# Performance work log

Measured on AMD Instinct MI355X. Metric: run time of the kernel, lower is better.

The kernel has to match this reference:

```python
import jax, jax.numpy as jnp
import numpy as np

LEAK = 0.01  # torch LeakyReLU default negative_slope

def lrelu(x):
    return jnp.where(x >= 0, x, LEAK * x)

def edge_conv(x, src, dst, ea, W1, b1, W2, b2):
    # message: cat(x_i=target, x_j=source, edge_attr) -> Linear -> LeakyReLU -> Linear
    m = jnp.concatenate([x[dst], x[src], ea], axis=1)          # [E, 2F+Fe]
    h = lrelu(m @ W1 + b1) @ W2 + b2                            # [E, H]
    n = x.shape[0]
    agg = jnp.full((n, h.shape[1]), jnp.inf, h.dtype).at[dst].min(h)  # scatter-min at target
    return jnp.where(jnp.isfinite(agg), agg, jnp.zeros_like(agg))     # empty nodes -> 0


def setup_inputs() -> dict:
    key = jax.random.key(0)
    ks = jax.random.split(key, 20)
    B, N, E = 4, 20000, 640000
    NF, AD, EF, H = 2, 1, 1, 8
    inp = {
        "node_features": jax.random.randint(ks[0], (B, N, NF), 0, 10, dtype=jnp.int32),
        "actions": jax.random.normal(ks[1], (B, N), dtype=jnp.float32),
        "edge_index": jax.random.randint(ks[2], (B, 2, E), 0, N, dtype=jnp.int64),
        "edge_features": jax.random.normal(ks[3], (B, E, EF), dtype=jnp.float32),
    }
    d0 = NF + AD  # 3
    def lin(k, fin, fout):
        s = 1.0 / np.sqrt(fin)
        k1, k2 = jax.random.split(k)
        return (jax.random.uniform(k1, (fin, fout), jnp.float32, -s, s),
                jax.random.uniform(k2, (fout,), jnp.float32, -s, s))
    inp["c1_W1"], inp["c1_b1"] = lin(ks[4], 2 * d0 + EF, H)
    inp["c1_W2"], inp["c1_b2"] = lin(ks[5], H, H)
    inp["c2_W1"], inp["c2_b1"] = lin(ks[6], 2 * H + 1, H)
    inp["c2_W2"], inp["c2_b2"] = lin(ks[7], H, H)
    inp["c3_W1"], inp["c3_b1"] = lin(ks[8], 2 * H + 1, H)
    inp["c3_W2"], inp["c3_b2"] = lin(ks[9], H, H)
    inp["lin_W"], inp["lin_b"] = lin(ks[10], d0 + H, 1)
    return inp


def reference(node_features, actions, edge_index, edge_features,
              c1_W1, c1_b1, c1_W2, c1_b2,
              c2_W1, c2_b1, c2_W2, c2_b2,
              c3_W1, c3_b1, c3_W2, c3_b2,
              lin_W, lin_b):
    # x = int(node_features) concat actions  -> float
    x0 = jnp.concatenate([node_features.astype(jnp.int32).astype(jnp.float32),
                          actions[..., None]], axis=-1)  # [B,N,3]

    def per_graph(x0g, eig, eag):
        src, dst = eig[0], eig[1]  # flow source_to_target: x_j=src, x_i=dst
        h = lrelu(edge_conv(x0g, src, dst, eag, c1_W1, c1_b1, c1_W2, c1_b2))
        h = lrelu(edge_conv(h, src, dst, eag, c2_W1, c2_b1, c2_W2, c2_b2))
        h = lrelu(edge_conv(h, src, dst, eag, c3_W1, c3_b1, c3_W2, c3_b2))
        xc = jnp.concatenate([x0g, h], axis=1)  # [N, 3+8]
        return jnp.sum(xc, axis=0)              # sum-pool over nodes

    pooled = jax.vmap(per_graph)(x0, edge_index, edge_features)  # [B, 11]
    return pooled @ lin_W + lin_b  # [B, 1]
```

## Files before the change

### kernel.cpp

```cpp
#include <hip/hip_runtime.h>

#define LEAK 0.01f
#define BS 128
#define PCHUNK 8192
#define PT 512
#define CT 512
#define MAXNB 1024

__device__ __forceinline__ float lrelu(float v) {
    return v >= 0.f ? v : LEAK * v;
}

__device__ __forceinline__ unsigned int fmin_encode(float x) {
    unsigned int u = __float_as_uint(x);
    return (u & 0x80000000u) ? ~u : (u | 0x80000000u);
}
__device__ __forceinline__ float fmin_decode(unsigned int k) {
    unsigned int u = (k & 0x80000000u) ? (k ^ 0x80000000u) : ~k;
    return __uint_as_float(u);
}

__device__ __forceinline__ void block_add(float c, float* dst) {
    __shared__ float wsum[8];
#pragma unroll
    for (int off = 32; off > 0; off >>= 1) c += __shfl_down(c, off, 64);
    int lane = threadIdx.x & 63;
    int wave = threadIdx.x >> 6;
    if (lane == 0) wsum[wave] = c;
    __syncthreads();
    if (threadIdx.x == 0) {
        float s = 0.f;
        int nw = blockDim.x >> 6;
        for (int w = 0; w < nw; ++w) s += wsum[w];
        atomicAdd(dst, s);
    }
}

__global__ __launch_bounds__(256) void init_pre1_kernel(
    const int* __restrict__ nf, const float* __restrict__ act,
    const float* __restrict__ W1, const float* __restrict__ b1,
    const float* __restrict__ lw, const float* __restrict__ lb,
    float* __restrict__ a1, float* __restrict__ a2,
    float* __restrict__ out, int N) {
    int b = blockIdx.y;
    int n = blockIdx.x * 256 + threadIdx.x;
    float c = 0.f;
    if (n < N) {
        size_t i = (size_t)b * N + n;
        float x0 = (float)nf[i * 2 + 0];
        float x1 = (float)nf[i * 2 + 1];
        float x2 = act[i];
        float v1[8], v2[8];
#pragma unroll
        for (int j = 0; j < 8; ++j) {
            v1[j] = b1[j] + x0 * W1[0 * 8 + j] + x1 * W1[1 * 8 + j] + x2 * W1[2 * 8 + j];
            v2[j] =         x0 * W1[3 * 8 + j] + x1 * W1[4 * 8 + j] + x2 * W1[5 * 8 + j];
        }
        float4* o1 = (float4*)(a1 + i * 8);
        float4* o2 = (float4*)(a2 + i * 8);
        o1[0] = make_float4(v1[0], v1[1], v1[2], v1[3]);
        o1[1] = make_float4(v1[4], v1[5], v1[6], v1[7]);
        o2[0] = make_float4(v2[0], v2[1], v2[2], v2[3]);
        o2[1] = make_float4(v2[4], v2[5], v2[6], v2[7]);
        c = x0 * lw[0] + x1 * lw[1] + x2 * lw[2];
        if (n == 0) c += lb[0];
    }
    block_add(c, &out[b]);
}


__global__ __launch_bounds__(PT) void bucket_hist_kernel(
    const int* __restrict__ ei, int* __restrict__ bcnt, int E, int NB) {
    __shared__ int lc[MAXNB];
    int b = blockIdx.y;
    int t = threadIdx.x;
    for (int i = t; i < NB; i += PT) lc[i] = 0;
    __syncthreads();
    int e0 = blockIdx.x * PCHUNK;
    int end = min(e0 + PCHUNK, E);
    const int* drow = ei + (size_t)b * 2 * E + E;
    for (int e = e0 + t; e < end; e += PT)
        atomicAdd(&lc[drow[e] >> 7], 1);
    __syncthreads();
    for (int i = t; i < NB; i += PT)
        if (lc[i]) atomicAdd(&bcnt[b * NB + i], lc[i]);
}

__global__ __launch_bounds__(1024) void bucket_scan_kernel(
    const int* __restrict__ bcnt, int* __restrict__ base,
    int* __restrict__ fill, int TB) {
    __shared__ int ts[1024];
    int t = threadIdx.x;
    int i0 = 2 * t, i1 = 2 * t + 1;
    int v0 = (i0 < TB) ? bcnt[i0] : 0;
    int v1 = (i1 < TB) ? bcnt[i1] : 0;
    int s = v0 + v1;
    ts[t] = s;
    __syncthreads();
    int incl = s;
    for (int off = 1; off < 1024; off <<= 1) {
        int add = (t >= off) ? ts[t - off] : 0;
        __syncthreads();
        incl += add;
        ts[t] = incl;
        __syncthreads();
    }
    int ex = incl - s;
    if (i0 < TB) { base[i0] = ex; fill[i0] = ex; }
    if (i1 < TB) { base[i1] = ex + v0; fill[i1] = ex + v0; }
    if (t == 0) base[TB] = ts[1023];
}

__global__ __launch_bounds__(PT) void part_kernel(
    const int* __restrict__ ei, const float* __restrict__ ea,
    int* __restrict__ fill, int2* __restrict__ pairs, int E, int NB) {
    __shared__ int lc[MAXNB];
    __shared__ int lbase[MAXNB];
    int b = blockIdx.y;
    int t = threadIdx.x;
    for (int i = t; i < NB; i += PT) lc[i] = 0;
    __syncthreads();
    int e0 = blockIdx.x * PCHUNK;
    int end = min(e0 + PCHUNK, E);
    const int* srow = ei + (size_t)b * 2 * E;
    const int* drow = srow + E;
    int pk[PCHUNK / PT];
#pragma unroll
    for (int j = 0; j < PCHUNK / PT; ++j) {
        int e = e0 + j * PT + t;
        int p = -1;
        if (e < end) {
            int d = drow[e];
            int bin = d >> 7;
            int r = atomicAdd(&lc[bin], 1);
            p = bin | ((d & 127) << 10) | (r << 17);
        }
        pk[j] = p;
    }
    __syncthreads();
    for (int i = t; i < NB; i += PT) {
        int c = lc[i];
        lbase[i] = c ? atomicAdd(&fill[b * NB + i], c) : 0;
    }
    __syncthreads();
#pragma unroll
    for (int j = 0; j < PCHUNK / PT; ++j) {
        int e = e0 + j * PT + t;
        if (e < end) {
            int p = pk[j];
            int bin = p & 1023;
            int dl = (p >> 10) & 127;
            int r = p >> 17;
            pairs[lbase[bin] + r] =
                make_int2(srow[e] | (dl << 16), __float_as_int(ea[(size_t)b * E + e]));
        }
    }
}


__device__ __forceinline__ void conv_edges(
    const float* __restrict__ a2g, const float* we, const float* bb,
    const float* __restrict__ W2, const int2* __restrict__ pairs,
    int k0, int k1, const float* __restrict__ a1s, unsigned int* __restrict__ acc) {
    int t = threadIdx.x;
    for (int k = k0 + t; k < k1; k += 2 * CT) {
        int2 p0 = pairs[k];
        bool has1 = (k + CT < k1);
        int2 p1 = has1 ? pairs[k + CT] : p0;
        const float4* q0 = (const float4*)(a2g + (size_t)(p0.x & 0xFFFF) * 8);
        float4 lo0 = q0[0], hi0 = q0[1];
        const float4* q1 = (const float4*)(a2g + (size_t)(p1.x & 0xFFFF) * 8);
        float4 lo1 = q1[0], hi1 = q1[1];
#pragma unroll
        for (int which = 0; which < 2; ++which) {
            if (which == 1 && !has1) break;
            int dl = ((which ? p1.x : p0.x) >> 16) & 127;
            float eav = __int_as_float(which ? p1.y : p0.y);
            float4 lo = which ? lo1 : lo0;
            float4 hi = which ? hi1 : hi0;
            float h1[8];
            h1[0] = a1s[dl * 9 + 0] + lo.x; h1[1] = a1s[dl * 9 + 1] + lo.y;
            h1[2] = a1s[dl * 9 + 2] + lo.z; h1[3] = a1s[dl * 9 + 3] + lo.w;
            h1[4] = a1s[dl * 9 + 4] + hi.x; h1[5] = a1s[dl * 9 + 5] + hi.y;
            h1[6] = a1s[dl * 9 + 6] + hi.z; h1[7] = a1s[dl * 9 + 7] + hi.w;
#pragma unroll
            for (int j = 0; j < 8; ++j) {
                h1[j] = fmaf(eav, we[j], h1[j]);
                h1[j] = lrelu(h1[j]);
            }
            float h2[8];
#pragma unroll
            for (int j = 0; j < 8; ++j) h2[j] = bb[j];
#pragma unroll
            for (int kk = 0; kk < 8; ++kk) {
                float hk = h1[kk];
#pragma unroll
                for (int j = 0; j < 8; ++j) h2[j] = fmaf(hk, W2[kk * 8 + j], h2[j]);
            }
#pragma unroll
            for (int j = 0; j < 8; ++j)
                atomicMin(&acc[dl * 9 + j], fmin_encode(h2[j]));
        }
    }
}

__global__ __launch_bounds__(CT) void conv_mid_kernel(
    const float* __restrict__ a1, const float* __restrict__ a2,
    const float* __restrict__ w1e, const float* __restrict__ W2,
    const float* __restrict__ b2,
    const float* __restrict__ nW1, const float* __restrict__ nb1,
    const int* __restrict__ base, const int2* __restrict__ pairs,
    float* __restrict__ na1, float* __restrict__ na2, int N, int NB) {
    __shared__ float a1s[BS * 9];
    __shared__ unsigned int acc[BS * 9];
    int b = blockIdx.y;
    int bkt = b * NB + blockIdx.x;
    int n0 = blockIdx.x << 7;
    int nCnt = min(BS, N - n0);
    int t = threadIdx.x;
    size_t gn0 = ((size_t)b * N + n0) * 8;

    for (int i = t; i < nCnt * 8; i += CT)
        a1s[(i >> 3) * 9 + (i & 7)] = a1[gn0 + i];
    for (int i = t; i < BS * 9; i += CT) acc[i] = 0xFFFFFFFFu;
    float we[8], bb[8];
#pragma unroll
    for (int j = 0; j < 8; ++j) { we[j] = w1e[j]; bb[j] = b2[j]; }
    __syncthreads();

    conv_edges(a2 + (size_t)b * N * 8, we, bb, W2, pairs, base[bkt], base[bkt + 1],
               a1s, acc);
    __syncthreads();

    for (int i = t; i < nCnt * 8; i += CT) {
        float v = fmin_decode(acc[(i >> 3) * 9 + (i & 7)]);
        unsigned int u = __float_as_uint(v);
        if ((u & 0x7F800000u) == 0x7F800000u) v = 0.f;
        a1s[(i >> 3) * 9 + (i & 7)] = lrelu(v);
    }
    __syncthreads();

    int node = t >> 1, half = t & 1;
    if (node < nCnt) {
        float h[8];
#pragma unroll
        for (int j = 0; j < 8; ++j) h[j] = a1s[node * 9 + j];
        float v[8];
#pragma unroll
        for (int j = 0; j < 8; ++j) v[j] = half ? 0.f : nb1[j];
        const float* Wbase = nW1 + (half ? 64 : 0);
#pragma unroll
        for (int k = 0; k < 8; ++k) {
            float hk = h[k];
#pragma unroll
            for (int j = 0; j < 8; ++j) v[j] = fmaf(hk, Wbase[k * 8 + j], v[j]);
        }
        float* dst = (half ? na2 : na1) + gn0 + (size_t)node * 8;
        float4* o = (float4*)dst;
        o[0] = make_float4(v[0], v[1], v[2], v[3]);
        o[1] = make_float4(v[4], v[5], v[6], v[7]);
    }
}

__global__ __launch_bounds__(CT) void conv_final_kernel(
    const float* __restrict__ a1, const float* __restrict__ a2,
    const float* __restrict__ w1e, const float* __restrict__ W2,
    const float* __restrict__ b2, const float* __restrict__ lw,
    const int* __restrict__ base, const int2* __restrict__ pairs,
    float* __restrict__ out, int N, int NB) {
    __shared__ float a1s[BS * 9];
    __shared__ unsigned int acc[BS * 9];
    int b = blockIdx.y;
    int bkt = b * NB + blockIdx.x;
    int n0 = blockIdx.x << 7;
    int nCnt = min(BS, N - n0);
    int t = threadIdx.x;
    size_t gn0 = ((size_t)b * N + n0) * 8;

    for (int i = t; i < nCnt * 8; i += CT)
        a1s[(i >> 3) * 9 + (i & 7)] = a1[gn0 + i];
    for (int i = t; i < BS * 9; i += CT) acc[i] = 0xFFFFFFFFu;
    float we[8], bb[8];
#pragma unroll
    for (int j = 0; j < 8; ++j) { we[j] = w1e[j]; bb[j] = b2[j]; }
    __syncthreads();

    conv_edges(a2 + (size_t)b * N * 8, we, bb, W2, pairs, base[bkt], base[bkt + 1],
               a1s, acc);
    __syncthreads();

    float c = 0.f;
    if (t < nCnt) {
#pragma unroll
        for (int j = 0; j < 8; ++j) {
            float v = fmin_decode(acc[t * 9 + j]);
            unsigned int u = __float_as_uint(v);
            if ((u & 0x7F800000u) == 0x7F800000u) v = 0.f;
            c = fmaf(lrelu(v), lw[3 + j], c);
        }
    }
    __syncthreads();
    block_add(c, &out[b]);
}


__global__ __launch_bounds__(256) void node_init_kernel(
    const int* __restrict__ nf, const float* __restrict__ act,
    float* __restrict__ x0, int BN) {
    int tid = blockIdx.x * blockDim.x + threadIdx.x;
    if (tid >= BN) return;
    x0[tid * 3 + 0] = (float)nf[tid * 2 + 0];
    x0[tid * 3 + 1] = (float)nf[tid * 2 + 1];
    x0[tid * 3 + 2] = act[tid];
}

template <int D>
__global__ __launch_bounds__(256) void edge_conv_kernel(
    const float* __restrict__ x, const int* __restrict__ ei,
    const float* __restrict__ ea,
    const float* __restrict__ W1, const float* __restrict__ b1,
    const float* __restrict__ W2, const float* __restrict__ b2,
    unsigned int* __restrict__ agg, int E, int N, int B) {
    int tid = blockIdx.x * blockDim.x + threadIdx.x;
    if (tid >= B * E) return;
    int b = tid / E;
    int e = tid - b * E;
    const int* eb = ei + (size_t)b * 2 * E;
    int s = eb[e];
    int d = eb[E + e];
    const float* xi = x + ((size_t)b * N + d) * D;
    const float* xj = x + ((size_t)b * N + s) * D;
    constexpr int M = 2 * D + 1;
    float m[M];
#pragma unroll
    for (int k = 0; k < D; ++k) { m[k] = xi[k]; m[D + k] = xj[k]; }
    m[2 * D] = ea[(size_t)b * E + e];
    float h1[8];
#pragma unroll
    for (int j = 0; j < 8; ++j) h1[j] = b1[j];
#pragma unroll
    for (int k = 0; k < M; ++k) {
        float mk = m[k];
#pragma unroll
        for (int j = 0; j < 8; ++j) h1[j] = fmaf(mk, W1[k * 8 + j], h1[j]);
    }
#pragma unroll
    for (int j = 0; j < 8; ++j) h1[j] = lrelu(h1[j]);
    float h2[8];
#pragma unroll
    for (int j = 0; j < 8; ++j) h2[j] = b2[j];
#pragma unroll
    for (int k = 0; k < 8; ++k) {
        float hk = h1[k];
#pragma unroll
        for (int j = 0; j < 8; ++j) h2[j] = fmaf(hk, W2[k * 8 + j], h2[j]);
    }
    unsigned int* ag = agg + ((size_t)b * N + d) * 8;
#pragma unroll
    for (int j = 0; j < 8; ++j) atomicMin(&ag[j], fmin_encode(h2[j]));
}

__global__ __launch_bounds__(256) void finalize_kernel(
    unsigned int* __restrict__ agg, int total) {
    int tid = blockIdx.x * blockDim.x + threadIdx.x;
    if (tid >= total) return;
    float v = fmin_decode(agg[tid]);
    unsigned int u = __float_as_uint(v);
    if ((u & 0x7F800000u) == 0x7F800000u) v = 0.f;
    ((float*)agg)[tid] = lrelu(v);
}

__global__ __launch_bounds__(256) void pool_kernel(
    const float* __restrict__ x0, const float* __restrict__ h,
    const float* __restrict__ lw, const float* __restrict__ lb,
    float* __restrict__ out, int N) {
    int b = blockIdx.y;
    int n = blockIdx.x * blockDim.x + threadIdx.x;
    float c = 0.f;
    if (n < N) {
        const float* x = x0 + ((size_t)b * N + n) * 3;
        const float* hh = h + ((size_t)b * N + n) * 8;
        c = x[0] * lw[0] + x[1] * lw[1] + x[2] * lw[2];
#pragma unroll
        for (int k = 0; k < 8; ++k) c = fmaf(hh[k], lw[3 + k], c);
        if (n == 0) c += lb[0];
    }
    block_add(c, &out[b]);
}


static inline size_t align256(size_t x) { return (x + 255) & ~(size_t)255; }

extern "C" void kernel_launch(void* const* d_in, const int* in_sizes, int n_in,
                              void* d_out, int out_size, void* d_ws, size_t ws_size,
                              hipStream_t stream) {
    const int B = 4;
    const int N = in_sizes[1] / B;
    const int E = in_sizes[2] / (2 * B);

    const int*   nf  = (const int*)d_in[0];
    const float* act = (const float*)d_in[1];
    const int*   ei  = (const int*)d_in[2];
    const float* ea  = (const float*)d_in[3];
    const float* c1_W1 = (const float*)d_in[4];
    const float* c1_b1 = (const float*)d_in[5];
    const float* c1_W2 = (const float*)d_in[6];
    const float* c1_b2 = (const float*)d_in[7];
    const float* c2_W1 = (const float*)d_in[8];
    const float* c2_b1 = (const float*)d_in[9];
    const float* c2_W2 = (const float*)d_in[10];
    const float* c2_b2 = (const float*)d_in[11];
    const float* c3_W1 = (const float*)d_in[12];
    const float* c3_b1 = (const float*)d_in[13];
    const float* c3_W2 = (const float*)d_in[14];
    const float* c3_b2 = (const float*)d_in[15];
    const float* lw    = (const float*)d_in[16];
    const float* lb    = (const float*)d_in[17];
    float* out = (float*)d_out;

    const int BN = B * N;
    const int BE = B * E;
    const int NB = (N + BS - 1) / BS;
    const int TB = B * NB;
    const int CPG = (E + PCHUNK - 1) / PCHUNK;

    char* ws = (char*)d_ws;
    size_t off = 0;
    float* a1A  = (float*)(ws + off);  off += align256((size_t)BN * 8 * 4);
    float* a2A  = (float*)(ws + off);  off += align256((size_t)BN * 8 * 4);
    float* a1B  = (float*)(ws + off);  off += align256((size_t)BN * 8 * 4);
    float* a2B  = (float*)(ws + off);  off += align256((size_t)BN * 8 * 4);
    int* bcnt   = (int*)(ws + off);    off += align256((size_t)TB * 4);
    int* base   = (int*)(ws + off);    off += align256((size_t)(TB + 1) * 4);
    int* fill   = (int*)(ws + off);    off += align256((size_t)TB * 4);
    int2* pairs = (int2*)(ws + off);   off += align256((size_t)BE * 8);
    float* x0   = (float*)(ws + off);  off += align256((size_t)BN * 3 * 4);
    const bool useFast = (off <= ws_size) && (NB <= MAXNB) && (TB <= 2048) &&
                         (N <= 65536);

    hipMemsetAsync(out, 0, (size_t)B * sizeof(float), stream);

    if (useFast) {
        dim3 egrid(CPG, B);
        dim3 igrid((N + 255) / 256, B);
        dim3 cgrid(NB, B);

        hipMemsetAsync(bcnt, 0, (size_t)TB * 4, stream);
        init_pre1_kernel<<<igrid, 256, 0, stream>>>(nf, act, c1_W1, c1_b1,
                                                    lw, lb, a1A, a2A, out, N);
        bucket_hist_kernel<<<egrid, PT, 0, stream>>>(ei, bcnt, E, NB);
        bucket_scan_kernel<<<1, 1024, 0, stream>>>(bcnt, base, fill, TB);
        part_kernel<<<egrid, PT, 0, stream>>>(ei, ea, fill, pairs, E, NB);

        conv_mid_kernel<<<cgrid, CT, 0, stream>>>(
            a1A, a2A, c1_W1 + 6 * 8, c1_W2, c1_b2, c2_W1, c2_b1,
            base, pairs, a1B, a2B, N, NB);
        conv_mid_kernel<<<cgrid, CT, 0, stream>>>(
            a1B, a2B, c2_W1 + 16 * 8, c2_W2, c2_b2, c3_W1, c3_b1,
            base, pairs, a1A, a2A, N, NB);
        conv_final_kernel<<<cgrid, CT, 0, stream>>>(
            a1A, a2A, c3_W1 + 16 * 8, c3_W2, c3_b2, lw,
            base, pairs, out, N, NB);
    } else {
        const int egrid = (BE + 255) / 256;
        const int aggTotal = BN * 8;
        const int agrid = (aggTotal + 255) / 256;
        const size_t aggBytes = (size_t)aggTotal * 4;
        unsigned int* uA = (unsigned int*)a1A;
        unsigned int* uB = (unsigned int*)a1B;

        node_init_kernel<<<(BN + 255) / 256, 256, 0, stream>>>(nf, act, x0, BN);

        hipMemsetAsync(uA, 0xFF, aggBytes, stream);
        edge_conv_kernel<3><<<egrid, 256, 0, stream>>>(
            x0, ei, ea, c1_W1, c1_b1, c1_W2, c1_b2, uA, E, N, B);
        finalize_kernel<<<agrid, 256, 0, stream>>>(uA, aggTotal);

        hipMemsetAsync(uB, 0xFF, aggBytes, stream);
        edge_conv_kernel<8><<<egrid, 256, 0, stream>>>(
            (const float*)uA, ei, ea, c2_W1, c2_b1, c2_W2, c2_b2, uB, E, N, B);
        finalize_kernel<<<agrid, 256, 0, stream>>>(uB, aggTotal);

        hipMemsetAsync(uA, 0xFF, aggBytes, stream);
        edge_conv_kernel<8><<<egrid, 256, 0, stream>>>(
            (const float*)uB, ei, ea, c3_W1, c3_b1, c3_W2, c3_b2, uA, E, N, B);
        finalize_kernel<<<agrid, 256, 0, stream>>>(uA, aggTotal);

        dim3 pgrid((N + 255) / 256, B);
        pool_kernel<<<pgrid, 256, 0, stream>>>(x0, (const float*)uA, lw, lb, out, N);
    }
}
```

Before: 223.8 us.

## Replace global bucket sort with per-chunk local partition and offset tables

Drops the global histogram, scan and atomic-fill passes. Each partition block now sorts its edge chunk locally by destination bin and writes per-chunk bin offsets. The conv kernels then walk the matching run in each of the CPG chunks, one wave per chunk. This removes two kernel launches, a memset and the global atomics, at the cost of fragmented, short reads in the three conv kernels, with many lanes idle on short runs.

```diff
diff --git a/kernel.cpp b/kernel.cpp
--- a/kernel.cpp
+++ b/kernel.cpp
@@ -6,6 +6,7 @@
 #define PT 512
 #define CT 512
 #define MAXNB 1024
+#define CPGMAX 256
 
 __device__ __forceinline__ float lrelu(float v) {
     return v >= 0.f ? v : LEAK * v;
@@ -68,62 +69,24 @@
     block_add(c, &out[b]);
 }
 
-
-__global__ __launch_bounds__(PT) void bucket_hist_kernel(
-    const int* __restrict__ ei, int* __restrict__ bcnt, int E, int NB) {
+__global__ __launch_bounds__(PT) void part_kernel(
+    const int* __restrict__ ei, const float* __restrict__ ea,
+    int2* __restrict__ pairs, int* __restrict__ ofs,
+    int E, int NB, int CPG) {
     __shared__ int lc[MAXNB];
+    __shared__ int lofs[MAXNB + 1];
+    __shared__ int ts[PT];
     int b = blockIdx.y;
+    int c = blockIdx.x;
     int t = threadIdx.x;
     for (int i = t; i < NB; i += PT) lc[i] = 0;
     __syncthreads();
-    int e0 = blockIdx.x * PCHUNK;
-    int end = min(e0 + PCHUNK, E);
-    const int* drow = ei + (size_t)b * 2 * E + E;
-    for (int e = e0 + t; e < end; e += PT)
-        atomicAdd(&lc[drow[e] >> 7], 1);
-    __syncthreads();
-    for (int i = t; i < NB; i += PT)
-        if (lc[i]) atomicAdd(&bcnt[b * NB + i], lc[i]);
-}
-
-__global__ __launch_bounds__(1024) void bucket_scan_kernel(
-    const int* __restrict__ bcnt, int* __restrict__ base,
-    int* __restrict__ fill, int TB) {
-    __shared__ int ts[1024];
-    int t = threadIdx.x;
-    int i0 = 2 * t, i1 = 2 * t + 1;
-    int v0 = (i0 < TB) ? bcnt[i0] : 0;
-    int v1 = (i1 < TB) ? bcnt[i1] : 0;
-    int s = v0 + v1;
-    ts[t] = s;
-    __syncthreads();
-    int incl = s;
-    for (int off = 1; off < 1024; off <<= 1) {
-        int add = (t >= off) ? ts[t - off] : 0;
-        __syncthreads();
-        incl += add;
-        ts[t] = incl;
-        __syncthreads();
-    }
-    int ex = incl - s;
-    if (i0 < TB) { base[i0] = ex; fill[i0] = ex; }
-    if (i1 < TB) { base[i1] = ex + v0; fill[i1] = ex + v0; }
-    if (t == 0) base[TB] = ts[1023];
-}
-
-__global__ __launch_bounds__(PT) void part_kernel(
-    const int* __restrict__ ei, const float* __restrict__ ea,
-    int* __restrict__ fill, int2* __restrict__ pairs, int E, int NB) {
-    __shared__ int lc[MAXNB];
-    __shared__ int lbase[MAXNB];
-    int b = blockIdx.y;
-    int t = threadIdx.x;
-    for (int i = t; i < NB; i += PT) lc[i] = 0;
-    __syncthreads();
-    int e0 = blockIdx.x * PCHUNK;
+
+    int e0 = c * PCHUNK;
     int end = min(e0 + PCHUNK, E);
     const int* srow = ei + (size_t)b * 2 * E;
     const int* drow = srow + E;
+
     int pk[PCHUNK / PT];
 #pragma unroll
     for (int j = 0; j < PCHUNK / PT; ++j) {
@@ -138,11 +101,36 @@
         pk[j] = p;
     }
     __syncthreads();
-    for (int i = t; i < NB; i += PT) {
-        int c = lc[i];
-        lbase[i] = c ? atomicAdd(&fill[b * NB + i], c) : 0;
-    }
-    __syncthreads();
+
+    int bin0 = 2 * t, bin1 = 2 * t + 1;
+    int v0 = (bin0 < NB) ? lc[bin0] : 0;
+    int v1 = (bin1 < NB) ? lc[bin1] : 0;
+    int s = v0 + v1;
+    ts[t] = s;
+    __syncthreads();
+    int incl = s;
+    for (int off = 1; off < PT; off <<= 1) {
+        int add = (t >= off) ? ts[t - off] : 0;
+        __syncthreads();
+        incl += add;
+        ts[t] = incl;
+        __syncthreads();
+    }
+    int ex = incl - s;
+    if (bin0 < NB) lofs[bin0] = ex;
+    if (bin1 < NB) lofs[bin1] = ex + v0;
+    if (t == PT - 1) lofs[NB] = incl;
+    __syncthreads();
+
+    int* og = ofs + ((size_t)b * CPG + c) * (NB + 1);
+    for (int i = t; i <= NB; i += PT) {
+        int v = lofs[i];
+        og[i] = v;
+        if (i < NB) lc[i] = v;
+    }
+    __syncthreads();
+
+    size_t pbase = (size_t)b * E + e0;
 #pragma unroll
     for (int j = 0; j < PCHUNK / PT; ++j) {
         int e = e0 + j * PT + t;
@@ -151,56 +139,67 @@
             int bin = p & 1023;
             int dl = (p >> 10) & 127;
             int r = p >> 17;
-            pairs[lbase[bin] + r] =
+            int pos = lc[bin] + r;
+            pairs[pbase + pos] =
                 make_int2(srow[e] | (dl << 16), __float_as_int(ea[(size_t)b * E + e]));
         }
     }
 }
 
 
-__device__ __forceinline__ void conv_edges(
+__device__ __forceinline__ void conv_edge_body(
     const float* __restrict__ a2g, const float* we, const float* bb,
-    const float* __restrict__ W2, const int2* __restrict__ pairs,
-    int k0, int k1, const float* __restrict__ a1s, unsigned int* __restrict__ acc) {
+    const float* __restrict__ W2, int2 p,
+    const float* __restrict__ a1s, unsigned int* __restrict__ acc) {
+    int srcn = p.x & 0xFFFF;
+    int dl = (p.x >> 16) & 127;
+    float eav = __int_as_float(p.y);
+    const float4* q = (const float4*)(a2g + (size_t)srcn * 8);
+    float4 lo = q[0], hi = q[1];
+    float h1[8];
+    h1[0] = a1s[dl * 9 + 0] + lo.x; h1[1] = a1s[dl * 9 + 1] + lo.y;
+    h1[2] = a1s[dl * 9 + 2] + lo.z; h1[3] = a1s[dl * 9 + 3] + lo.w;
+    h1[4] = a1s[dl * 9 + 4] + hi.x; h1[5] = a1s[dl * 9 + 5] + hi.y;
+    h1[6] = a1s[dl * 9 + 6] + hi.z; h1[7] = a1s[dl * 9 + 7] + hi.w;
+#pragma unroll
+    for (int j = 0; j < 8; ++j) {
+        h1[j] = fmaf(eav, we[j], h1[j]);
+        h1[j] = lrelu(h1[j]);
+    }
+    float h2[8];
+#pragma unroll
+    for (int j = 0; j < 8; ++j) h2[j] = bb[j];
+#pragma unroll
+    for (int kk = 0; kk < 8; ++kk) {
+        float hk = h1[kk];
+#pragma unroll
+        for (int j = 0; j < 8; ++j) h2[j] = fmaf(hk, W2[kk * 8 + j], h2[j]);
+    }
+#pragma unroll
+    for (int j = 0; j < 8; ++j)
+        atomicMin(&acc[dl * 9 + j], fmin_encode(h2[j]));
+}
+
+__device__ __forceinline__ void conv_edges_runs(
+    const float* __restrict__ a2g, const float* we, const float* bb,
+    const float* __restrict__ W2, const int2* __restrict__ pairsg,
+    const int* __restrict__ ofsg, int bin, int NB, int CPG,
+    const float* __restrict__ a1s, unsigned int* __restrict__ acc,
+    int* __restrict__ rs, int* __restrict__ re) {
     int t = threadIdx.x;
-    for (int k = k0 + t; k < k1; k += 2 * CT) {
-        int2 p0 = pairs[k];
-        bool has1 = (k + CT < k1);
-        int2 p1 = has1 ? pairs[k + CT] : p0;
-        const float4* q0 = (const float4*)(a2g + (size_t)(p0.x & 0xFFFF) * 8);
-        float4 lo0 = q0[0], hi0 = q0[1];
-        const float4* q1 = (const float4*)(a2g + (size_t)(p1.x & 0xFFFF) * 8);
-        float4 lo1 = q1[0], hi1 = q1[1];
-#pragma unroll
-        for (int which = 0; which < 2; ++which) {
-            if (which == 1 && !has1) break;
-            int dl = ((which ? p1.x : p0.x) >> 16) & 127;
-            float eav = __int_as_float(which ? p1.y : p0.y);
-            float4 lo = which ? lo1 : lo0;
-            float4 hi = which ? hi1 : hi0;
-            float h1[8];
-            h1[0] = a1s[dl * 9 + 0] + lo.x; h1[1] = a1s[dl * 9 + 1] + lo.y;
-            h1[2] = a1s[dl * 9 + 2] + lo.z; h1[3] = a1s[dl * 9 + 3] + lo.w;
-            h1[4] = a1s[dl * 9 + 4] + hi.x; h1[5] = a1s[dl * 9 + 5] + hi.y;
-            h1[6] = a1s[dl * 9 + 6] + hi.z; h1[7] = a1s[dl * 9 + 7] + hi.w;
-#pragma unroll
-            for (int j = 0; j < 8; ++j) {
-                h1[j] = fmaf(eav, we[j], h1[j]);
-                h1[j] = lrelu(h1[j]);
-            }
-            float h2[8];
-#pragma unroll
-            for (int j = 0; j < 8; ++j) h2[j] = bb[j];
-#pragma unroll
-            for (int kk = 0; kk < 8; ++kk) {
-                float hk = h1[kk];
-#pragma unroll
-                for (int j = 0; j < 8; ++j) h2[j] = fmaf(hk, W2[kk * 8 + j], h2[j]);
-            }
-#pragma unroll
-            for (int j = 0; j < 8; ++j)
-                atomicMin(&acc[dl * 9 + j], fmin_encode(h2[j]));
-        }
+    for (int c = t; c < CPG; c += CT) {
+        const int* o = ofsg + (size_t)c * (NB + 1) + bin;
+        rs[c] = o[0];
+        re[c] = o[1];
+    }
+    __syncthreads();
+    int wave = t >> 6, lane = t & 63;
+    const int nw = CT >> 6;
+    for (int c = wave; c < CPG; c += nw) {
+        int cb = c * PCHUNK;
+        int k1 = cb + re[c];
+        for (int k = cb + rs[c] + lane; k < k1; k += 64)
+            conv_edge_body(a2g, we, bb, W2, pairsg[k], a1s, acc);
     }
 }
 
@@ -209,13 +208,16 @@
     const float* __restrict__ w1e, const float* __restrict__ W2,
     const float* __restrict__ b2,
     const float* __restrict__ nW1, const float* __restrict__ nb1,
-    const int* __restrict__ base, const int2* __restrict__ pairs,
-    float* __restrict__ na1, float* __restrict__ na2, int N, int NB) {
+    const int* __restrict__ ofs, const int2* __restrict__ pairs,
+    float* __restrict__ na1, float* __restrict__ na2,
+    int N, int NB, int CPG, int E) {
     __shared__ float a1s[BS * 9];
     __shared__ unsigned int acc[BS * 9];
+    __shared__ int rs[CPGMAX];
+    __shared__ int re[CPGMAX];
     int b = blockIdx.y;
-    int bkt = b * NB + blockIdx.x;
-    int n0 = blockIdx.x << 7;
+    int bin = blockIdx.x;
+    int n0 = bin << 7;
     int nCnt = min(BS, N - n0);
     int t = threadIdx.x;
     size_t gn0 = ((size_t)b * N + n0) * 8;
@@ -228,8 +230,9 @@
     for (int j = 0; j < 8; ++j) { we[j] = w1e[j]; bb[j] = b2[j]; }
     __syncthreads();
 
-    conv_edges(a2 + (size_t)b * N * 8, we, bb, W2, pairs, base[bkt], base[bkt + 1],
-               a1s, acc);
+    conv_edges_runs(a2 + (size_t)b * N * 8, we, bb, W2,
+                    pairs + (size_t)b * E, ofs + (size_t)b * CPG * (NB + 1),
+                    bin, NB, CPG, a1s, acc, rs, re);
     __syncthreads();
 
     for (int i = t; i < nCnt * 8; i += CT) {
@@ -266,13 +269,15 @@
     const float* __restrict__ a1, const float* __restrict__ a2,
     const float* __restrict__ w1e, const float* __restrict__ W2,
     const float* __restrict__ b2, const float* __restrict__ lw,
-    const int* __restrict__ base, const int2* __restrict__ pairs,
-    float* __restrict__ out, int N, int NB) {
+    const int* __restrict__ ofs, const int2* __restrict__ pairs,
+    float* __restrict__ out, int N, int NB, int CPG, int E) {
     __shared__ float a1s[BS * 9];
     __shared__ unsigned int acc[BS * 9];
+    __shared__ int rs[CPGMAX];
+    __shared__ int re[CPGMAX];
     int b = blockIdx.y;
-    int bkt = b * NB + blockIdx.x;
-    int n0 = blockIdx.x << 7;
+    int bin = blockIdx.x;
+    int n0 = bin << 7;
     int nCnt = min(BS, N - n0);
     int t = threadIdx.x;
     size_t gn0 = ((size_t)b * N + n0) * 8;
@@ -285,8 +290,9 @@
     for (int j = 0; j < 8; ++j) { we[j] = w1e[j]; bb[j] = b2[j]; }
     __syncthreads();
 
-    conv_edges(a2 + (size_t)b * N * 8, we, bb, W2, pairs, base[bkt], base[bkt + 1],
-               a1s, acc);
+    conv_edges_runs(a2 + (size_t)b * N * 8, we, bb, W2,
+                    pairs + (size_t)b * E, ofs + (size_t)b * CPG * (NB + 1),
+                    bin, NB, CPG, a1s, acc, rs, re);
     __syncthreads();
 
     float c = 0.f;
@@ -421,7 +427,6 @@
     const int BN = B * N;
     const int BE = B * E;
     const int NB = (N + BS - 1) / BS;
-    const int TB = B * NB;
     const int CPG = (E + PCHUNK - 1) / PCHUNK;
 
     char* ws = (char*)d_ws;
@@ -430,37 +435,32 @@
     float* a2A  = (float*)(ws + off);  off += align256((size_t)BN * 8 * 4);
     float* a1B  = (float*)(ws + off);  off += align256((size_t)BN * 8 * 4);
     float* a2B  = (float*)(ws + off);  off += align256((size_t)BN * 8 * 4);
-    int* bcnt   = (int*)(ws + off);    off += align256((size_t)TB * 4);
-    int* base   = (int*)(ws + off);    off += align256((size_t)(TB + 1) * 4);
-    int* fill   = (int*)(ws + off);    off += align256((size_t)TB * 4);
+    int* ofs    = (int*)(ws + off);    off += align256((size_t)B * CPG * (NB + 1) * 4);
     int2* pairs = (int2*)(ws + off);   off += align256((size_t)BE * 8);
     float* x0   = (float*)(ws + off);  off += align256((size_t)BN * 3 * 4);
-    const bool useFast = (off <= ws_size) && (NB <= MAXNB) && (TB <= 2048) &&
+    const bool useFast = (off <= ws_size) && (NB <= MAXNB) && (CPG <= CPGMAX) &&
                          (N <= 65536);
 
     hipMemsetAsync(out, 0, (size_t)B * sizeof(float), stream);
 
     if (useFast) {
-        dim3 egrid(CPG, B);
+        dim3 pgrid(CPG, B);
         dim3 igrid((N + 255) / 256, B);
         dim3 cgrid(NB, B);
 
-        hipMemsetAsync(bcnt, 0, (size_t)TB * 4, stream);
         init_pre1_kernel<<<igrid, 256, 0, stream>>>(nf, act, c1_W1, c1_b1,
                                                     lw, lb, a1A, a2A, out, N);
-        bucket_hist_kernel<<<egrid, PT, 0, stream>>>(ei, bcnt, E, NB);
-        bucket_scan_kernel<<<1, 1024, 0, stream>>>(bcnt, base, fill, TB);
-        part_kernel<<<egrid, PT, 0, stream>>>(ei, ea, fill, pairs, E, NB);
+        part_kernel<<<pgrid, PT, 0, stream>>>(ei, ea, pairs, ofs, E, NB, CPG);
 
         conv_mid_kernel<<<cgrid, CT, 0, stream>>>(
             a1A, a2A, c1_W1 + 6 * 8, c1_W2, c1_b2, c2_W1, c2_b1,
-            base, pairs, a1B, a2B, N, NB);
+            ofs, pairs, a1B, a2B, N, NB, CPG, E);
         conv_mid_kernel<<<cgrid, CT, 0, stream>>>(
             a1B, a2B, c2_W1 + 16 * 8, c2_W2, c2_b2, c3_W1, c3_b1,
-            base, pairs, a1A, a2A, N, NB);
+            ofs, pairs, a1A, a2A, N, NB, CPG, E);
         conv_final_kernel<<<cgrid, CT, 0, stream>>>(
             a1A, a2A, c3_W1 + 16 * 8, c3_W2, c3_b2, lw,
-            base, pairs, out, N, NB);
+            ofs, pairs, out, N, NB, CPG, E);
     } else {
         const int egrid = (BE + 255) / 256;
         const int aggTotal = BN * 8;
@@ -486,7 +486,7 @@
             (const float*)uB, ei, ea, c3_W1, c3_b1, c3_W2, c3_b2, uA, E, N, B);
         finalize_kernel<<<agrid, 256, 0, stream>>>(uA, aggTotal);
 
-        dim3 pgrid((N + 255) / 256, B);
-        pool_kernel<<<pgrid, 256, 0, stream>>>(x0, (const float*)uA, lw, lb, out, N);
-    }
-}
+        dim3 plgrid((N + 255) / 256, B);
+        pool_kernel<<<plgrid, 256, 0, stream>>>(x0, (const float*)uA, lw, lb, out, N);
+    }
+}
```

Measured after the change: 218.7 us. 2.3% less time.
